# Kernel tuning notes

Hardware: AMD Instinct MI355X
Metric: run time of the kernel (lower is better)

## Reference

```python
import jax, jax.numpy as jnp
import numpy as np

B, T, D, H, E = 4, 2048, 1024, 4096, 8
TOP_K = 2


def setup_inputs() -> dict:
    key = jax.random.key(0)
    k0, k1, k2, k3, k4, k5 = jax.random.split(key, 6)
    x = jax.random.normal(k0, (B, T, D), dtype=jnp.float32)
    noise = jax.random.normal(k1, (B, T, E), dtype=jnp.float32)
    # torch Linear weights are [out, in]; y = x @ W.T
    Wr = jax.random.normal(k2, (E, D), dtype=jnp.float32) * 0.02  # route_linear
    Wn = jax.random.normal(k3, (E, D), dtype=jnp.float32) * 0.02  # noise_linear
    # expert weights stacked: fc1 [E, D, H] (already transposed), fc2 [E, H, D]
    W1 = jax.random.normal(k4, (E, D, H), dtype=jnp.float32) * 0.02
    W2 = jax.random.normal(k5, (E, H, D), dtype=jnp.float32) * 0.02
    return {"x": x, "noise": noise, "Wr": Wr, "Wn": Wn, "W1": W1, "W2": W2}


def reference(x, noise, Wr, Wn, W1, W2):
    n_experts = Wr.shape[0]
    # --- noisy top-k router ---
    logits = jnp.einsum('btd,ed->bte', x, Wr)
    noise_logits = jnp.einsum('btd,ed->bte', x, Wn)
    noisy = logits + noise * jax.nn.softplus(noise_logits)          # [B,T,E]
    _, idx = jax.lax.top_k(noisy, TOP_K)                            # [B,T,k]
    sel = (idx[..., None] == jnp.arange(n_experts)).any(axis=-2)    # [B,T,E] bool
    sparse_logits = jnp.where(sel, noisy, -jnp.inf)
    gates = jax.nn.softmax(sparse_logits, axis=-1)                  # zero for non-selected
    # --- dispatch / expert FFN / combine ---
    # gate is exactly 0 for non-selected experts, so weighting the dense
    # per-expert output by gates reproduces the gather-GEMM-scatter math.
    out = jnp.zeros_like(x)
    for e in range(n_experts):  # small fixed expert count
        h = jnp.square(jax.nn.relu(x @ W1[e]))   # [B,T,H], relu(x)^2 activation
        out = out + gates[..., e:e + 1] * (h @ W2[e])
    return out
```

## Files before the change

### kernel.cpp

```cpp
#include <hip/hip_runtime.h>
#include <hip/hip_bf16.h>

#define NTOK 8192
#define DDIM 1024
#define HDIM 4096
#define NEXP 8
#define NSLOT (NTOK * 2)
#define MAXTILES 136

#define BM 128
#define BN 128
#define BK 32

typedef __attribute__((ext_vector_type(8))) short bfrag;
typedef __attribute__((ext_vector_type(4))) float f32x4;

__device__ __forceinline__ unsigned short f2bf(float f) {
  union { __hip_bfloat16 h; unsigned short u; } cv;
  cv.h = __float2bfloat16(f);
  return cv.u;
}

__device__ __forceinline__ void glds16(const unsigned short* g, unsigned short* l) {
  __builtin_amdgcn_global_load_lds(
      (const __attribute__((address_space(1))) unsigned int*)g,
      (__attribute__((address_space(3))) unsigned int*)l, 16, 0, 0);
}

#define WS_COUNTS      0UL
#define WS_CURSORS     256UL
#define WS_OFFSETS     512UL
#define WS_TABLE       1024UL
#define WS_TOKE        4096UL
#define WS_TOKG        69632UL
#define WS_SLOT_TOKEN  135168UL
#define WS_SLOT_GATE   200704UL
#define WS_XB          266240UL
#define WS_DYN         17043456UL

__global__ void cvt_x_kernel(const float* __restrict__ x,
                             unsigned short* __restrict__ xb, int n4) {
  int i = blockIdx.x * blockDim.x + threadIdx.x;
  if (i >= n4) return;
  float4 v = reinterpret_cast<const float4*>(x)[i];
  ushort4 u;
  u.x = f2bf(v.x); u.y = f2bf(v.y); u.z = f2bf(v.z); u.w = f2bf(v.w);
  reinterpret_cast<ushort4*>(xb)[i] = u;
}

__global__ void transpose_cvt_kernel(const float* __restrict__ in,
                                     unsigned short* __restrict__ out,
                                     int Rsub, int in_rstride,
                                     size_t in_estride, size_t out_estride) {
  __shared__ float tile[32][33];
  int b = blockIdx.z;
  int r0 = blockIdx.y * 32, c0 = blockIdx.x * 32;
  const float* src = in + (size_t)b * in_estride;
  unsigned short* dst = out + (size_t)b * out_estride;
  int tc = threadIdx.x & 31, tr = threadIdx.x >> 5;
#pragma unroll
  for (int i = 0; i < 4; i++)
    tile[tr + 8 * i][tc] = src[(size_t)(r0 + tr + 8 * i) * in_rstride + (c0 + tc)];
  __syncthreads();
#pragma unroll
  for (int i = 0; i < 4; i++)
    dst[(size_t)(c0 + tr + 8 * i) * Rsub + (r0 + tc)] = f2bf(tile[tc][tr + 8 * i]);
}

__global__ void router_kernel(const float* __restrict__ x,
                              const float* __restrict__ noise,
                              const float* __restrict__ Wr,
                              const float* __restrict__ Wn,
                              int* __restrict__ counts,
                              int* __restrict__ tok_e,
                              float* __restrict__ tok_g) {
  int tok = (int)((blockIdx.x * (size_t)blockDim.x + threadIdx.x) >> 6);
  int lane = threadIdx.x & 63;
  if (tok >= NTOK) return;
  const float* xrow = x + (size_t)tok * DDIM;

  float accR[NEXP], accN[NEXP];
#pragma unroll
  for (int e = 0; e < NEXP; e++) { accR[e] = 0.f; accN[e] = 0.f; }

  for (int j = 0; j < DDIM / 64; j++) {
    int d = lane + 64 * j;
    float xv = xrow[d];
#pragma unroll
    for (int e = 0; e < NEXP; e++) {
      accR[e] = fmaf(xv, Wr[e * DDIM + d], accR[e]);
      accN[e] = fmaf(xv, Wn[e * DDIM + d], accN[e]);
    }
  }
#pragma unroll
  for (int e = 0; e < NEXP; e++) {
    float r = accR[e], n = accN[e];
    for (int s = 32; s > 0; s >>= 1) { r += __shfl_xor(r, s); n += __shfl_xor(n, s); }
    accR[e] = r; accN[e] = n;
  }
  if (lane == 0) {
    float noisy[NEXP];
#pragma unroll
    for (int e = 0; e < NEXP; e++) {
      float nl = accN[e];
      float sp = (nl > 15.f) ? nl : log1pf(expf(nl));
      noisy[e] = accR[e] + noise[(size_t)tok * NEXP + e] * sp;
    }
    int i0 = 0;
#pragma unroll
    for (int e = 1; e < NEXP; e++) if (noisy[e] > noisy[i0]) i0 = e;
    int i1 = (i0 == 0) ? 1 : 0;
#pragma unroll
    for (int e = 0; e < NEXP; e++)
      if (e != i0 && noisy[e] > noisy[i1]) i1 = e;
    float ex = expf(noisy[i1] - noisy[i0]);
    float denom = 1.f + ex;
    tok_e[tok * 2 + 0] = i0; tok_e[tok * 2 + 1] = i1;
    tok_g[tok * 2 + 0] = 1.f / denom; tok_g[tok * 2 + 1] = ex / denom;
    atomicAdd(&counts[i0], 1);
    atomicAdd(&counts[i1], 1);
  }
}

__global__ void build_meta_kernel(const int* __restrict__ counts,
                                  int* __restrict__ offsets,
                                  int* __restrict__ cursors,
                                  int4* __restrict__ table) {
  if (threadIdx.x == 0) {
    int off = 0, nt = 0;
    for (int e = 0; e < NEXP; e++) {
      offsets[e] = off;
      cursors[e] = 0;
      int c = counts[e];
      for (int r = 0; r < c; r += BM) {
        int rows = c - r; if (rows > BM) rows = BM;
        table[nt++] = make_int4(e, off + r, rows, 0);
      }
      off += c;
    }
    offsets[NEXP] = off;
    for (; nt < MAXTILES; nt++) table[nt] = make_int4(-1, 0, 0, 0);
  }
}

__global__ void assign_slots_kernel(const int* __restrict__ tok_e,
                                    const float* __restrict__ tok_g,
                                    const int* __restrict__ offsets,
                                    int* __restrict__ cursors,
                                    int* __restrict__ slot_token,
                                    float* __restrict__ slot_gate) {
  int t = blockIdx.x * blockDim.x + threadIdx.x;
  if (t >= NTOK) return;
#pragma unroll
  for (int k = 0; k < 2; k++) {
    int e = tok_e[t * 2 + k];
    int pos = atomicAdd(&cursors[e], 1);
    int s = offsets[e] + pos;
    slot_token[s] = t;
    slot_gate[s] = tok_g[t * 2 + k];
  }
}

template <int MODE>
__global__ __launch_bounds__(256) void moe_gemm_kernel(
    const unsigned short* __restrict__ Amat,
    const unsigned short* __restrict__ Bmat,
    const int4* __restrict__ table,
    const int* __restrict__ slot_token,
    const float* __restrict__ slot_gate,
    unsigned short* __restrict__ hout,
    float* __restrict__ oout,
    int kd, int astride, int b_rstride, size_t b_estride, int hcur) {
  int4 te = table[blockIdx.y];
  int e = te.x;
  if (e < 0) return;
  int slot_base = te.y;
  int rows = te.z;
  int col0 = blockIdx.x * BN;

  __shared__ __align__(16) unsigned short As[BM][BK];
  __shared__ __align__(16) unsigned short Bs[BN][BK];

  int tid = threadIdx.x;
  int lane = tid & 63, wid = tid >> 6;
  int wr = wid >> 1, wc = wid & 1;

  int r0 = (wid * 2 + 0) * 16 + (lane >> 2);
  int r1 = (wid * 2 + 1) * 16 + (lane >> 2);
  int koff = (lane & 3) * 8;

  int s0 = slot_base + r0; if (s0 > NSLOT - 1) s0 = NSLOT - 1;
  int s1 = slot_base + r1; if (s1 > NSLOT - 1) s1 = NSLOT - 1;
  size_t arow0, arow1;
  if (MODE == 0) { arow0 = (size_t)slot_token[s0] * astride; arow1 = (size_t)slot_token[s1] * astride; }
  else           { arow0 = (size_t)s0 * astride;             arow1 = (size_t)s1 * astride; }
  const unsigned short* ag0 = Amat + arow0 + koff;
  const unsigned short* ag1 = Amat + arow1 + koff;
  const unsigned short* bbase = Bmat + (size_t)e * b_estride;
  const unsigned short* bg0 = bbase + (size_t)(col0 + r0) * b_rstride + koff;
  const unsigned short* bg1 = bbase + (size_t)(col0 + r1) * b_rstride + koff;

  unsigned short* la0 = &As[(wid * 2 + 0) * 16][0];
  unsigned short* la1 = &As[(wid * 2 + 1) * 16][0];
  unsigned short* lb0 = &Bs[(wid * 2 + 0) * 16][0];
  unsigned short* lb1 = &Bs[(wid * 2 + 1) * 16][0];

  f32x4 acc[4][4];
#pragma unroll
  for (int m = 0; m < 4; m++)
#pragma unroll
    for (int n = 0; n < 4; n++) acc[m][n] = (f32x4)(0.f);

  const int gk = (lane >> 4) * 8;
  const int rl = lane & 15;

  for (int k0 = 0; k0 < kd; k0 += BK) {
    __syncthreads();
    glds16(ag0 + k0, la0);
    glds16(ag1 + k0, la1);
    glds16(bg0 + k0, lb0);
    glds16(bg1 + k0, lb1);
    __syncthreads();

    bfrag af[4], bfr[4];
#pragma unroll
    for (int m = 0; m < 4; m++)
      af[m] = *reinterpret_cast<const bfrag*>(&As[wr * 64 + m * 16 + rl][gk]);
#pragma unroll
    for (int n = 0; n < 4; n++)
      bfr[n] = *reinterpret_cast<const bfrag*>(&Bs[wc * 64 + n * 16 + rl][gk]);
#pragma unroll
    for (int m = 0; m < 4; m++)
#pragma unroll
      for (int n = 0; n < 4; n++)
        acc[m][n] = __builtin_amdgcn_mfma_f32_16x16x32_bf16(af[m], bfr[n], acc[m][n], 0, 0, 0);
  }

  const int gi = lane >> 4, cl = lane & 15;
  if (MODE == 0) {
#pragma unroll
    for (int m = 0; m < 4; m++) {
#pragma unroll
      for (int rr = 0; rr < 4; rr++) {
        int row = wr * 64 + m * 16 + gi * 4 + rr;
        if (row < rows) {
          size_t base = (size_t)(slot_base + row) * hcur;
#pragma unroll
          for (int n = 0; n < 4; n++) {
            int col = col0 + wc * 64 + n * 16 + cl;
            float v = fmaxf(acc[m][n][rr], 0.f);
            hout[base + col] = f2bf(v * v);
          }
        }
      }
    }
  } else {
#pragma unroll
    for (int m = 0; m < 4; m++) {
#pragma unroll
      for (int rr = 0; rr < 4; rr++) {
        int row = wr * 64 + m * 16 + gi * 4 + rr;
        if (row < rows) {
          int slot = slot_base + row;
          int tok = slot_token[slot];
          float gv = slot_gate[slot];
          float* obase = oout + (size_t)tok * DDIM;
#pragma unroll
          for (int n = 0; n < 4; n++) {
            int col = col0 + wc * 64 + n * 16 + cl;
            atomicAdd(&obase[col], gv * acc[m][n][rr]);
          }
        }
      }
    }
  }
}

extern "C" void kernel_launch(void* const* d_in, const int* in_sizes, int n_in,
                              void* d_out, int out_size, void* d_ws, size_t ws_size,
                              hipStream_t stream) {
  const float* x     = (const float*)d_in[0];
  const float* noise = (const float*)d_in[1];
  const float* Wr    = (const float*)d_in[2];
  const float* Wn    = (const float*)d_in[3];
  const float* W1    = (const float*)d_in[4];
  const float* W2    = (const float*)d_in[5];
  float* out = (float*)d_out;
  char* ws = (char*)d_ws;

  int*   counts     = (int*)(ws + WS_COUNTS);
  int*   cursors    = (int*)(ws + WS_CURSORS);
  int*   offsets    = (int*)(ws + WS_OFFSETS);
  int4*  table      = (int4*)(ws + WS_TABLE);
  int*   tok_e      = (int*)(ws + WS_TOKE);
  float* tok_g      = (float*)(ws + WS_TOKG);
  int*   slot_token = (int*)(ws + WS_SLOT_TOKEN);
  float* slot_gate  = (float*)(ws + WS_SLOT_GATE);
  unsigned short* xb = (unsigned short*)(ws + WS_XB);

  (void)in_sizes; (void)n_in;

  int HC = 128;
  for (int cand = HDIM; cand >= 128; cand >>= 1) {
    if (WS_DYN + 65536ULL * (unsigned long long)cand <= (unsigned long long)ws_size) { HC = cand; break; }
  }
  unsigned short* W1Tc = (unsigned short*)(ws + WS_DYN);
  unsigned short* W2Tc = W1Tc + (size_t)NEXP * HC * DDIM;
  unsigned short* hbuf = W2Tc + (size_t)NEXP * DDIM * HC;

  hipMemsetAsync(ws + WS_COUNTS, 0, 64, stream);
  hipMemsetAsync(out, 0, (size_t)out_size * sizeof(float), stream);

  {
    int n4 = NTOK * DDIM / 4;
    cvt_x_kernel<<<(n4 + 255) / 256, 256, 0, stream>>>(x, xb, n4);
  }

  router_kernel<<<NTOK * 64 / 256, 256, 0, stream>>>(x, noise, Wr, Wn, counts, tok_e, tok_g);
  build_meta_kernel<<<1, 64, 0, stream>>>(counts, offsets, cursors, table);
  assign_slots_kernel<<<NTOK / 256, 256, 0, stream>>>(tok_e, tok_g, offsets, cursors,
                                                      slot_token, slot_gate);

  int nc = HDIM / HC;
  for (int c = 0; c < nc; ++c) {
    size_t hc0 = (size_t)c * HC;
    transpose_cvt_kernel<<<dim3(HC / 32, DDIM / 32, NEXP), 256, 0, stream>>>(
        W1 + hc0, W1Tc, DDIM, HDIM, (size_t)DDIM * HDIM, (size_t)HC * DDIM);
    transpose_cvt_kernel<<<dim3(DDIM / 32, HC / 32, NEXP), 256, 0, stream>>>(
        W2 + hc0 * DDIM, W2Tc, HC, DDIM, (size_t)HDIM * DDIM, (size_t)DDIM * HC);

    moe_gemm_kernel<0><<<dim3(HC / BN, MAXTILES), 256, 0, stream>>>(
        xb, W1Tc, table, slot_token, slot_gate, hbuf, nullptr,
        DDIM, DDIM, DDIM, (size_t)HC * DDIM, HC);
    moe_gemm_kernel<1><<<dim3(DDIM / BN, MAXTILES), 256, 0, stream>>>(
        hbuf, W2Tc, table, slot_token, slot_gate, nullptr, out,
        HC, HC, HC, (size_t)DDIM * HC, HC);
  }
}
```

Measured before the change: 1.098 ms.

## Double-buffer LDS in MoE GEMM and vectorize weight transpose with 64x64 tiles

The MoE GEMM kernel now keeps two LDS buffers and issues the async global-to-LDS loads for the next K tile before computing on the current one, leaving one barrier per iteration instead of two. This is meant to hide global load latency behind MFMA work, at the cost of doubling LDS use, which may lower occupancy. Separately, the weight transpose-convert kernel moves to 64x64 tiles with float4 reads and ushort4 writes to cut per-element memory transactions, using a 64x65 float tile in LDS.

```diff
diff --git a/kernel.cpp b/kernel.cpp
--- a/kernel.cpp
+++ b/kernel.cpp
@@ -48,23 +48,35 @@
   reinterpret_cast<ushort4*>(xb)[i] = u;
 }
 
-__global__ void transpose_cvt_kernel(const float* __restrict__ in,
-                                     unsigned short* __restrict__ out,
-                                     int Rsub, int in_rstride,
-                                     size_t in_estride, size_t out_estride) {
-  __shared__ float tile[32][33];
+__global__ __launch_bounds__(256) void transpose_cvt_kernel(
+    const float* __restrict__ in, unsigned short* __restrict__ out,
+    int Rsub, int in_rstride, size_t in_estride, size_t out_estride) {
+  __shared__ float tile[64][65];
   int b = blockIdx.z;
-  int r0 = blockIdx.y * 32, c0 = blockIdx.x * 32;
-  const float* src = in + (size_t)b * in_estride;
-  unsigned short* dst = out + (size_t)b * out_estride;
-  int tc = threadIdx.x & 31, tr = threadIdx.x >> 5;
-#pragma unroll
-  for (int i = 0; i < 4; i++)
-    tile[tr + 8 * i][tc] = src[(size_t)(r0 + tr + 8 * i) * in_rstride + (c0 + tc)];
+  int r0 = blockIdx.y * 64, c0 = blockIdx.x * 64;
+  const float* src = in + (size_t)b * in_estride + (size_t)r0 * in_rstride + c0;
+  unsigned short* dst = out + (size_t)b * out_estride + (size_t)c0 * Rsub + r0;
+  int t = threadIdx.x;
+  int lr = t >> 4;
+  int lc4 = (t & 15) * 4;
+#pragma unroll
+  for (int p = 0; p < 4; p++) {
+    int r = lr + p * 16;
+    float4 v = *reinterpret_cast<const float4*>(src + (size_t)r * in_rstride + lc4);
+    tile[r][lc4 + 0] = v.x; tile[r][lc4 + 1] = v.y;
+    tile[r][lc4 + 2] = v.z; tile[r][lc4 + 3] = v.w;
+  }
   __syncthreads();
 #pragma unroll
-  for (int i = 0; i < 4; i++)
-    dst[(size_t)(c0 + tr + 8 * i) * Rsub + (r0 + tc)] = f2bf(tile[tc][tr + 8 * i]);
+  for (int p = 0; p < 4; p++) {
+    int c = lr + p * 16;
+    ushort4 u;
+    u.x = f2bf(tile[lc4 + 0][c]);
+    u.y = f2bf(tile[lc4 + 1][c]);
+    u.z = f2bf(tile[lc4 + 2][c]);
+    u.w = f2bf(tile[lc4 + 3][c]);
+    *reinterpret_cast<ushort4*>(dst + (size_t)c * Rsub + lc4) = u;
+  }
 }
 
 __global__ void router_kernel(const float* __restrict__ x,
@@ -178,15 +190,15 @@
   int rows = te.z;
   int col0 = blockIdx.x * BN;
 
-  __shared__ __align__(16) unsigned short As[BM][BK];
-  __shared__ __align__(16) unsigned short Bs[BN][BK];
+  __shared__ __align__(16) unsigned short As[2][BM][BK];
+  __shared__ __align__(16) unsigned short Bs[2][BM][BK];
 
   int tid = threadIdx.x;
   int lane = tid & 63, wid = tid >> 6;
   int wr = wid >> 1, wc = wid & 1;
 
-  int r0 = (wid * 2 + 0) * 16 + (lane >> 2);
-  int r1 = (wid * 2 + 1) * 16 + (lane >> 2);
+  int r0 = wid * 32 + (lane >> 2);
+  int r1 = wid * 32 + 16 + (lane >> 2);
   int koff = (lane & 3) * 8;
 
   int s0 = slot_base + r0; if (s0 > NSLOT - 1) s0 = NSLOT - 1;
@@ -200,11 +212,6 @@
   const unsigned short* bg0 = bbase + (size_t)(col0 + r0) * b_rstride + koff;
   const unsigned short* bg1 = bbase + (size_t)(col0 + r1) * b_rstride + koff;
 
-  unsigned short* la0 = &As[(wid * 2 + 0) * 16][0];
-  unsigned short* la1 = &As[(wid * 2 + 1) * 16][0];
-  unsigned short* lb0 = &Bs[(wid * 2 + 0) * 16][0];
-  unsigned short* lb1 = &Bs[(wid * 2 + 1) * 16][0];
-
   f32x4 acc[4][4];
 #pragma unroll
   for (int m = 0; m < 4; m++)
@@ -214,26 +221,37 @@
   const int gk = (lane >> 4) * 8;
   const int rl = lane & 15;
 
-  for (int k0 = 0; k0 < kd; k0 += BK) {
-    __syncthreads();
-    glds16(ag0 + k0, la0);
-    glds16(ag1 + k0, la1);
-    glds16(bg0 + k0, lb0);
-    glds16(bg1 + k0, lb1);
-    __syncthreads();
-
+  int nt = kd / BK;
+  glds16(ag0, &As[0][wid * 32][0]);
+  glds16(ag1, &As[0][wid * 32 + 16][0]);
+  glds16(bg0, &Bs[0][wid * 32][0]);
+  glds16(bg1, &Bs[0][wid * 32 + 16][0]);
+  __syncthreads();
+
+  int cur = 0;
+  for (int t = 0; t < nt; ++t) {
+    if (t + 1 < nt) {
+      int nk = (t + 1) * BK;
+      int nxt = cur ^ 1;
+      glds16(ag0 + nk, &As[nxt][wid * 32][0]);
+      glds16(ag1 + nk, &As[nxt][wid * 32 + 16][0]);
+      glds16(bg0 + nk, &Bs[nxt][wid * 32][0]);
+      glds16(bg1 + nk, &Bs[nxt][wid * 32 + 16][0]);
+    }
     bfrag af[4], bfr[4];
 #pragma unroll
     for (int m = 0; m < 4; m++)
-      af[m] = *reinterpret_cast<const bfrag*>(&As[wr * 64 + m * 16 + rl][gk]);
+      af[m] = *reinterpret_cast<const bfrag*>(&As[cur][wr * 64 + m * 16 + rl][gk]);
 #pragma unroll
     for (int n = 0; n < 4; n++)
-      bfr[n] = *reinterpret_cast<const bfrag*>(&Bs[wc * 64 + n * 16 + rl][gk]);
+      bfr[n] = *reinterpret_cast<const bfrag*>(&Bs[cur][wc * 64 + n * 16 + rl][gk]);
 #pragma unroll
     for (int m = 0; m < 4; m++)
 #pragma unroll
       for (int n = 0; n < 4; n++)
         acc[m][n] = __builtin_amdgcn_mfma_f32_16x16x32_bf16(af[m], bfr[n], acc[m][n], 0, 0, 0);
+    __syncthreads();
+    cur ^= 1;
   }
 
   const int gi = lane >> 4, cl = lane & 15;
@@ -324,9 +342,9 @@
   int nc = HDIM / HC;
   for (int c = 0; c < nc; ++c) {
     size_t hc0 = (size_t)c * HC;
-    transpose_cvt_kernel<<<dim3(HC / 32, DDIM / 32, NEXP), 256, 0, stream>>>(
+    transpose_cvt_kernel<<<dim3(HC / 64, DDIM / 64, NEXP), 256, 0, stream>>>(
         W1 + hc0, W1Tc, DDIM, HDIM, (size_t)DDIM * HDIM, (size_t)HC * DDIM);
-    transpose_cvt_kernel<<<dim3(DDIM / 32, HC / 32, NEXP), 256, 0, stream>>>(
+    transpose_cvt_kernel<<<dim3(DDIM / 64, HC / 64, NEXP), 256, 0, stream>>>(
         W2 + hc0 * DDIM, W2Tc, HC, DDIM, (size_t)HDIM * DDIM, (size_t)DDIM * HC);
 
     moe_gemm_kernel<0><<<dim3(HC / BN, MAXTILES), 256, 0, stream>>>(
```

Result: faster. 1.077 ms (-2.0%).
